# Performance work log

Hardware: AMD Instinct MI355X
Metric: run time of the kernel (lower is better)

Reference implementation:

```python
import jax, jax.numpy as jnp
from jax import lax
import numpy as np

S, B, IN, H, OUT = 101, 16384, 9, 32, 3


def setup_inputs() -> dict:
    key = jax.random.key(0)
    ks = jax.random.split(key, 7)
    s = 1.0 / np.sqrt(H)  # PyTorch LSTM init scale
    return {
        "x": jax.random.normal(ks[0], (S, B, IN), jnp.float32),
        "W_ih": jax.random.uniform(ks[1], (4 * H, IN), jnp.float32, -s, s),
        "W_hh": jax.random.uniform(ks[2], (4 * H, H), jnp.float32, -s, s),
        "b_ih": jax.random.uniform(ks[3], (4 * H,), jnp.float32, -s, s),
        "b_hh": jax.random.uniform(ks[4], (4 * H,), jnp.float32, -s, s),
        "W_lin": jax.random.uniform(ks[5], (OUT, H * S), jnp.float32, -s, s),
        "b_lin": jax.random.uniform(ks[6], (OUT,), jnp.float32, -s, s),
    }


def reference(x, W_ih, W_hh, b_ih, b_hh, W_lin, b_lin):
    seq, batch, _ = x.shape
    hdim = W_hh.shape[1]
    # Precompute input projections for all timesteps: [S, B, 4H]
    x_proj = jnp.einsum('sbi,gi->sbg', x, W_ih) + b_ih + b_hh

    def step(carry, xp_t):
        h, c = carry
        gates = xp_t + h @ W_hh.T  # [B, 4H], PyTorch gate order i,f,g,o
        i, f, g, o = jnp.split(gates, 4, axis=-1)
        c = jax.nn.sigmoid(f) * c + jax.nn.sigmoid(i) * jnp.tanh(g)
        h = jax.nn.sigmoid(o) * jnp.tanh(c)
        return (h, c), h

    h0 = jnp.zeros((batch, hdim), x.dtype)
    (_, _), hs = lax.scan(step, (h0, h0), x_proj)  # hs: [S, B, H]
    # Faithful to the torch code: reshape seq-major output to (-1, H*S)
    flat = hs.reshape(-1, hdim * seq)  # [B, H*S] (seq/batch-interleaved rows)
    return flat @ W_lin.T + b_lin  # [B, OUT]
```

## Files before the change

kernel.cpp:

```cpp
#include <hip/hip_runtime.h>
#include <hip/hip_bf16.h>

#define SEQ   101
#define BATCH 16384
#define INP   9
#define HID   32
#define NOUT  3
#define HSlin 3232
#define SB    (SEQ * BATCH)

typedef __attribute__((ext_vector_type(8))) _Float16 half8;
typedef __attribute__((ext_vector_type(8))) short short8;
typedef __attribute__((ext_vector_type(4))) float f32x4;
typedef __attribute__((ext_vector_type(2))) float f32x2;
typedef __attribute__((ext_vector_type(4))) unsigned u32x4;

#define LOG2E   1.4426950408889634f
#define N2LOG2E (-2.8853900817779268f)

__device__ __forceinline__ unsigned pkh(float a, float b) {
    return __builtin_bit_cast(unsigned, __builtin_amdgcn_cvt_pkrtz(a, b));
}
__device__ __forceinline__ unsigned dpp8u(unsigned v) {
    return (unsigned)__builtin_amdgcn_mov_dpp((int)v, 0x128, 0xF, 0xF, true);
}
__device__ __forceinline__ float dpp8f(float v) {
    return __int_as_float(__builtin_amdgcn_mov_dpp(__float_as_int(v), 0x128, 0xF, 0xF, true));
}

__global__ void prep_kernel(const float* __restrict__ W_ih, const float* __restrict__ W_hh,
                            const float* __restrict__ b_ih, const float* __restrict__ b_hh,
                            unsigned short* __restrict__ whh16, unsigned short* __restrict__ wih16,
                            float* __restrict__ biasc) {
    int tid = threadIdx.x;
    int l   = tid & 63;
    int t   = tid >> 6;
    int row = l & 15;
    int g   = l >> 4;
    int gate = 16 * t + row;
    float sc = ((gate >> 5) == 2) ? (2.f * LOG2E) : LOG2E;
    for (int j = 0; j < 8; ++j) {
        int u = 4 * g + (j & 3) + 16 * (j >> 2);
        _Float16 wh = (_Float16)(W_hh[gate * HID + u] * sc);
        whh16[tid * 8 + j] = __builtin_bit_cast(unsigned short, wh);
        int k = 8 * g + j;
        _Float16 wi = (_Float16)((k < INP) ? (W_ih[gate * INP + k] * sc) : 0.f);
        wih16[tid * 8 + j] = __builtin_bit_cast(unsigned short, wi);
    }
    if (tid < 4 * HID) {
        float bs = ((tid >> 5) == 2) ? (2.f * LOG2E) : LOG2E;
        biasc[tid] = (b_ih[tid] + b_hh[tid]) * bs;
    }
}

template<bool PLANES>
__device__ __forceinline__ void emit_prev(float p0, float p1, float p2,
                                          unsigned psb, float* __restrict__ dataout,
                                          int lane, int cr) {
    p0 += dpp8f(p0);          p1 += dpp8f(p1);          p2 += dpp8f(p2);
    p0 += __shfl_xor(p0, 16); p1 += __shfl_xor(p1, 16); p2 += __shfl_xor(p2, 16);
    p0 += __shfl_xor(p0, 32); p1 += __shfl_xor(p1, 32); p2 += __shfl_xor(p2, 32);
    if (PLANES) {
        if (lane < 8) {
            unsigned blk = psb + (unsigned)lane;
            dataout[0 * SB + blk] = p0;
            dataout[1 * SB + blk] = p1;
            dataout[2 * SB + blk] = p2;
        }
    } else {
        unsigned blk  = psb + (unsigned)cr;
        unsigned r    = blk / 101u;
        unsigned rmin = psb / 101u;
        bool low = (r == rmin);
        float a0 = low ? p0 : 0.f, a1 = low ? p1 : 0.f, a2 = low ? p2 : 0.f;
        float d0 = low ? 0.f : p0, d1 = low ? 0.f : p1, d2 = low ? 0.f : p2;
#pragma unroll
        for (int m = 1; m < 8; m <<= 1) {
            a0 += __shfl_xor(a0, m); a1 += __shfl_xor(a1, m); a2 += __shfl_xor(a2, m);
            d0 += __shfl_xor(d0, m); d1 += __shfl_xor(d1, m); d2 += __shfl_xor(d2, m);
        }
        int anyhi = __any(!low && lane < 8);
        if (lane == 0) {
            atomicAdd(&dataout[rmin * 3 + 0], a0);
            atomicAdd(&dataout[rmin * 3 + 1], a1);
            atomicAdd(&dataout[rmin * 3 + 2], a2);
            if (anyhi) {
                atomicAdd(&dataout[(rmin + 1u) * 3 + 0], d0);
                atomicAdd(&dataout[(rmin + 1u) * 3 + 1], d1);
                atomicAdd(&dataout[(rmin + 1u) * 3 + 2], d2);
            }
        }
    }
}

template<bool PLANES>
__global__ __launch_bounds__(64, 2) void lstm_kernel(
    const float* __restrict__ x,
    const unsigned short* __restrict__ whh_g,
    const unsigned short* __restrict__ wih_g,
    const float* __restrict__ biasc,
    const float* __restrict__ W_lin,
    float* __restrict__ dataout)
{
    const int lane = threadIdx.x;
    const int c    = lane & 15;
    const int cr   = c & 7;
    const bool hi8 = (lane & 8) != 0;
    const int g    = lane >> 4;
    const int b0   = blockIdx.x * 8;
    const int b    = b0 + cr;

    half8 whh[8], xw[8];
    f32x4 biasv[8];
#pragma unroll
    for (int t = 0; t < 8; ++t) {
        whh[t] = __builtin_bit_cast(half8, *reinterpret_cast<const short8*>(whh_g + (t * 64 + lane) * 8));
        xw[t]  = __builtin_bit_cast(half8, *reinterpret_cast<const short8*>(wih_g + (t * 64 + lane) * 8));
        biasv[t] = *reinterpret_cast<const f32x4*>(biasc + 16 * t + 4 * g);
    }

    const bool g0 = (g == 0), g1 = (g == 1);

    f32x2 cs[2] = {{0.f, 0.f}, {0.f, 0.f}};
    f32x2 ho[2] = {{0.f, 0.f}, {0.f, 0.f}};
    u32x4 bhv = {0u, 0u, 0u, 0u};
    float xv[9];
    {
        const float* xp = x + (size_t)b * INP;
#pragma unroll
        for (int i = 0; i < 9; ++i) xv[i] = xp[i];
    }

    float pp0 = 0.f, pp1 = 0.f, pp2 = 0.f;
    unsigned psb = 0;

#pragma unroll 1
    for (int s = 0; s < SEQ; ++s) {
        unsigned blk  = (unsigned)s * BATCH + (unsigned)b;
        unsigned r    = blk / 101u;
        unsigned slot = blk - r * 101u;
        const float* wl = W_lin + slot * HID + 4 * g + (hi8 ? 16 : 0);
        float4 w0 = *(const float4*)(wl);
        float4 w1 = *(const float4*)(wl + HSlin);
        float4 w2 = *(const float4*)(wl + 2 * HSlin);

        short8 xa;
        {
            unsigned x01 = pkh(xv[0], xv[1]), x23 = pkh(xv[2], xv[3]);
            unsigned x45 = pkh(xv[4], xv[5]), x67 = pkh(xv[6], xv[7]);
            unsigned x8z = pkh(xv[8], 0.f);
            u32x4 xt;
            xt[0] = g0 ? x01 : (g1 ? x8z : 0u);
            xt[1] = g0 ? x23 : 0u;
            xt[2] = g0 ? x45 : 0u;
            xt[3] = g0 ? x67 : 0u;
            xa = __builtin_bit_cast(short8, xt);
        }
        half8 bh = __builtin_bit_cast(half8, bhv);

        f32x4 acc[8];
#pragma unroll
        for (int t = 0; t < 8; ++t) {
            acc[t] = __builtin_amdgcn_mfma_f32_16x16x32_f16(xw[t], __builtin_bit_cast(half8, xa), biasv[t], 0, 0, 0);
            acc[t] = __builtin_amdgcn_mfma_f32_16x16x32_f16(whh[t], bh, acc[t], 0, 0, 0);
        }
        if (s > 0) emit_prev<PLANES>(pp0, pp1, pp2, psb, dataout, lane, cr);

        float xn[9];
        if (s < SEQ - 1) {
            const float* xpn = x + ((size_t)(s + 1) * BATCH + b) * INP;
#pragma unroll
            for (int i = 0; i < 9; ++i) xn[i] = xpn[i];
        }

        f32x4 aI = hi8 ? acc[1] : acc[0];
        f32x4 aF = hi8 ? acc[3] : acc[2];
        f32x4 aG = hi8 ? acc[5] : acc[4];
        f32x4 aO = hi8 ? acc[7] : acc[6];
#pragma unroll
        for (int p = 0; p < 2; ++p) {
            f32x2 ef = {__builtin_amdgcn_exp2f(-aF[2*p]), __builtin_amdgcn_exp2f(-aF[2*p+1])};
            f32x2 ei = {__builtin_amdgcn_exp2f(-aI[2*p]), __builtin_amdgcn_exp2f(-aI[2*p+1])};
            f32x2 eg = {__builtin_amdgcn_exp2f(-aG[2*p]), __builtin_amdgcn_exp2f(-aG[2*p+1])};
            f32x2 pf = ef + 1.f;
            f32x2 A  = (ei + 1.f) * (eg + 1.f);
            f32x2 num = cs[p] * A + (1.f - eg) * pf;
            f32x2 den = pf * A;
            f32x2 rd = {__builtin_amdgcn_rcpf(den.x), __builtin_amdgcn_rcpf(den.y)};
            f32x2 cn = num * rd;
            cs[p] = cn;
            f32x2 eo = {__builtin_amdgcn_exp2f(-aO[2*p]), __builtin_amdgcn_exp2f(-aO[2*p+1])};
            f32x2 ec = {__builtin_amdgcn_exp2f(cn.x * N2LOG2E), __builtin_amdgcn_exp2f(cn.y * N2LOG2E)};
            f32x2 dd = (eo + 1.f) * (ec + 1.f);
            f32x2 rh = {__builtin_amdgcn_rcpf(dd.x), __builtin_amdgcn_rcpf(dd.y)};
            ho[p] = (1.f - ec) * rh;
        }
        {
            unsigned oh01 = pkh(ho[0].x, ho[0].y);
            unsigned oh23 = pkh(ho[1].x, ho[1].y);
            unsigned th01 = dpp8u(oh01), th23 = dpp8u(oh23);
            bhv[0] = hi8 ? th01 : oh01;  bhv[1] = hi8 ? th23 : oh23;
            bhv[2] = hi8 ? oh01 : th01;  bhv[3] = hi8 ? oh23 : th23;
        }
        if (s < SEQ - 1) {
#pragma unroll
            for (int i = 0; i < 9; ++i) xv[i] = xn[i];
        }

        pp0 = w0.x * ho[0].x + w0.y * ho[0].y + w0.z * ho[1].x + w0.w * ho[1].y;
        pp1 = w1.x * ho[0].x + w1.y * ho[0].y + w1.z * ho[1].x + w1.w * ho[1].y;
        pp2 = w2.x * ho[0].x + w2.y * ho[0].y + w2.z * ho[1].x + w2.w * ho[1].y;
        psb = (unsigned)s * BATCH + (unsigned)b0;
    }
    emit_prev<PLANES>(pp0, pp1, pp2, psb, dataout, lane, cr);
}

__global__ void finalize_planes(const float* __restrict__ planes, const float* __restrict__ b_lin,
                                float* __restrict__ out) {
    int wid = (blockIdx.x * blockDim.x + threadIdx.x) >> 6;
    int l   = threadIdx.x & 63;
    float v[3];
#pragma unroll
    for (int o = 0; o < 3; ++o) {
        const float* p = planes + (size_t)o * SB + (size_t)wid * 101;
        float t = p[l] + ((l < 37) ? p[l + 64] : 0.f);
#pragma unroll
        for (int m = 1; m < 64; m <<= 1) t += __shfl_xor(t, m);
        v[o] = t;
    }
    if (l == 0) {
        out[wid * 3 + 0] = v[0] + b_lin[0];
        out[wid * 3 + 1] = v[1] + b_lin[1];
        out[wid * 3 + 2] = v[2] + b_lin[2];
    }
}

__global__ void finalize_acc(const float* __restrict__ acc, const float* __restrict__ b_lin,
                             float* __restrict__ out) {
    int i = blockIdx.x * blockDim.x + threadIdx.x;
    if (i < BATCH * NOUT) {
        int r = i / 3;
        int o = i - r * 3;
        out[i] = acc[i] + b_lin[o];
    }
}

extern "C" void kernel_launch(void* const* d_in, const int* in_sizes, int n_in,
                              void* d_out, int out_size, void* d_ws, size_t ws_size,
                              hipStream_t stream) {
    const float* x     = (const float*)d_in[0];
    const float* W_ih  = (const float*)d_in[1];
    const float* W_hh  = (const float*)d_in[2];
    const float* b_ih  = (const float*)d_in[3];
    const float* b_hh  = (const float*)d_in[4];
    const float* W_lin = (const float*)d_in[5];
    const float* b_lin = (const float*)d_in[6];
    float* out = (float*)d_out;

    unsigned short* whh16 = (unsigned short*)d_ws;
    unsigned short* wih16 = whh16 + 4096;
    float* biasc = (float*)(wih16 + 4096);
    float* data  = (float*)((char*)d_ws + 25600);

    size_t need_planes = 25600 + (size_t)3 * SB * sizeof(float);
    bool planes = ws_size >= need_planes;

    hipLaunchKernelGGL(prep_kernel, dim3(1), dim3(512), 0, stream,
                       W_ih, W_hh, b_ih, b_hh, whh16, wih16, biasc);
    if (planes) {
        hipLaunchKernelGGL((lstm_kernel<true>), dim3(BATCH / 8), dim3(64), 0, stream,
                           x, whh16, wih16, biasc, W_lin, data);
        hipLaunchKernelGGL(finalize_planes, dim3(BATCH / 4), dim3(256), 0, stream,
                           data, b_lin, out);
    } else {
        hipMemsetAsync(data, 0, 49160 * sizeof(float), stream);
        hipLaunchKernelGGL((lstm_kernel<false>), dim3(BATCH / 8), dim3(64), 0, stream,
                           x, whh16, wih16, biasc, W_lin, data);
        hipLaunchKernelGGL(finalize_acc, dim3((BATCH * NOUT + 255) / 256), dim3(256), 0, stream,
                           data, b_lin, out);
    }
}
```

Measured before the change: 114.2 us.

## Process 16 batch columns per wave, dropping DPP half-swap of hidden state

Each wave now owns 16 batch elements instead of 8, using the full MFMA N dimension. Each lane computes gate nonlinearities for both hidden halves, so the DPP lane swaps for the h vector and the partial-sum reduction go away. The launch grid halves and launch bounds drop to one wave per SIMD to allow more registers. In exchange, per-lane elementwise work doubles and fewer waves are available to hide the serial recurrence latency.

```diff
diff --git a/kernel.cpp b/kernel.cpp
--- a/kernel.cpp
+++ b/kernel.cpp
@@ -20,12 +20,6 @@
 
 __device__ __forceinline__ unsigned pkh(float a, float b) {
     return __builtin_bit_cast(unsigned, __builtin_amdgcn_cvt_pkrtz(a, b));
-}
-__device__ __forceinline__ unsigned dpp8u(unsigned v) {
-    return (unsigned)__builtin_amdgcn_mov_dpp((int)v, 0x128, 0xF, 0xF, true);
-}
-__device__ __forceinline__ float dpp8f(float v) {
-    return __int_as_float(__builtin_amdgcn_mov_dpp(__float_as_int(v), 0x128, 0xF, 0xF, true));
 }
 
 __global__ void prep_kernel(const float* __restrict__ W_ih, const float* __restrict__ W_hh,
@@ -56,30 +50,29 @@
 template<bool PLANES>
 __device__ __forceinline__ void emit_prev(float p0, float p1, float p2,
                                           unsigned psb, float* __restrict__ dataout,
-                                          int lane, int cr) {
-    p0 += dpp8f(p0);          p1 += dpp8f(p1);          p2 += dpp8f(p2);
+                                          int lane, int c) {
     p0 += __shfl_xor(p0, 16); p1 += __shfl_xor(p1, 16); p2 += __shfl_xor(p2, 16);
     p0 += __shfl_xor(p0, 32); p1 += __shfl_xor(p1, 32); p2 += __shfl_xor(p2, 32);
     if (PLANES) {
-        if (lane < 8) {
+        if (lane < 16) {
             unsigned blk = psb + (unsigned)lane;
             dataout[0 * SB + blk] = p0;
             dataout[1 * SB + blk] = p1;
             dataout[2 * SB + blk] = p2;
         }
     } else {
-        unsigned blk  = psb + (unsigned)cr;
+        unsigned blk  = psb + (unsigned)c;
         unsigned r    = blk / 101u;
         unsigned rmin = psb / 101u;
         bool low = (r == rmin);
         float a0 = low ? p0 : 0.f, a1 = low ? p1 : 0.f, a2 = low ? p2 : 0.f;
         float d0 = low ? 0.f : p0, d1 = low ? 0.f : p1, d2 = low ? 0.f : p2;
 #pragma unroll
-        for (int m = 1; m < 8; m <<= 1) {
+        for (int m = 1; m < 16; m <<= 1) {
             a0 += __shfl_xor(a0, m); a1 += __shfl_xor(a1, m); a2 += __shfl_xor(a2, m);
             d0 += __shfl_xor(d0, m); d1 += __shfl_xor(d1, m); d2 += __shfl_xor(d2, m);
         }
-        int anyhi = __any(!low && lane < 8);
+        int anyhi = __any(!low && lane < 16);
         if (lane == 0) {
             atomicAdd(&dataout[rmin * 3 + 0], a0);
             atomicAdd(&dataout[rmin * 3 + 1], a1);
@@ -94,7 +87,7 @@
 }
 
 template<bool PLANES>
-__global__ __launch_bounds__(64, 2) void lstm_kernel(
+__global__ __launch_bounds__(64, 1) void lstm_kernel(
     const float* __restrict__ x,
     const unsigned short* __restrict__ whh_g,
     const unsigned short* __restrict__ wih_g,
@@ -104,11 +97,9 @@
 {
     const int lane = threadIdx.x;
     const int c    = lane & 15;
-    const int cr   = c & 7;
-    const bool hi8 = (lane & 8) != 0;
     const int g    = lane >> 4;
-    const int b0   = blockIdx.x * 8;
-    const int b    = b0 + cr;
+    const int b0   = blockIdx.x * 16;
+    const int b    = b0 + c;
 
     half8 whh[8], xw[8];
     f32x4 biasv[8];
@@ -121,8 +112,8 @@
 
     const bool g0 = (g == 0), g1 = (g == 1);
 
-    f32x2 cs[2] = {{0.f, 0.f}, {0.f, 0.f}};
-    f32x2 ho[2] = {{0.f, 0.f}, {0.f, 0.f}};
+    f32x2 cs[4] = {{0.f,0.f},{0.f,0.f},{0.f,0.f},{0.f,0.f}};
+    f32x2 hp[4] = {{0.f,0.f},{0.f,0.f},{0.f,0.f},{0.f,0.f}};
     u32x4 bhv = {0u, 0u, 0u, 0u};
     float xv[9];
     {
@@ -139,10 +130,13 @@
         unsigned blk  = (unsigned)s * BATCH + (unsigned)b;
         unsigned r    = blk / 101u;
         unsigned slot = blk - r * 101u;
-        const float* wl = W_lin + slot * HID + 4 * g + (hi8 ? 16 : 0);
-        float4 w0 = *(const float4*)(wl);
-        float4 w1 = *(const float4*)(wl + HSlin);
-        float4 w2 = *(const float4*)(wl + 2 * HSlin);
+        const float* wl = W_lin + slot * HID + 4 * g;
+        float4 w0a = *(const float4*)(wl);
+        float4 w0b = *(const float4*)(wl + 16);
+        float4 w1a = *(const float4*)(wl + HSlin);
+        float4 w1b = *(const float4*)(wl + HSlin + 16);
+        float4 w2a = *(const float4*)(wl + 2 * HSlin);
+        float4 w2b = *(const float4*)(wl + 2 * HSlin + 16);
 
         short8 xa;
         {
@@ -164,7 +158,7 @@
             acc[t] = __builtin_amdgcn_mfma_f32_16x16x32_f16(xw[t], __builtin_bit_cast(half8, xa), biasv[t], 0, 0, 0);
             acc[t] = __builtin_amdgcn_mfma_f32_16x16x32_f16(whh[t], bh, acc[t], 0, 0, 0);
         }
-        if (s > 0) emit_prev<PLANES>(pp0, pp1, pp2, psb, dataout, lane, cr);
+        if (s > 0) emit_prev<PLANES>(pp0, pp1, pp2, psb, dataout, lane, c);
 
         float xn[9];
         if (s < SEQ - 1) {
@@ -173,15 +167,16 @@
             for (int i = 0; i < 9; ++i) xn[i] = xpn[i];
         }
 
-        f32x4 aI = hi8 ? acc[1] : acc[0];
-        f32x4 aF = hi8 ? acc[3] : acc[2];
-        f32x4 aG = hi8 ? acc[5] : acc[4];
-        f32x4 aO = hi8 ? acc[7] : acc[6];
-#pragma unroll
-        for (int p = 0; p < 2; ++p) {
-            f32x2 ef = {__builtin_amdgcn_exp2f(-aF[2*p]), __builtin_amdgcn_exp2f(-aF[2*p+1])};
-            f32x2 ei = {__builtin_amdgcn_exp2f(-aI[2*p]), __builtin_amdgcn_exp2f(-aI[2*p+1])};
-            f32x2 eg = {__builtin_amdgcn_exp2f(-aG[2*p]), __builtin_amdgcn_exp2f(-aG[2*p+1])};
+#pragma unroll
+        for (int p = 0; p < 4; ++p) {
+            const int ht = p >> 1, q0 = 2 * (p & 1);
+            f32x2 aI = {acc[0 + ht][q0], acc[0 + ht][q0 + 1]};
+            f32x2 aF = {acc[2 + ht][q0], acc[2 + ht][q0 + 1]};
+            f32x2 aG = {acc[4 + ht][q0], acc[4 + ht][q0 + 1]};
+            f32x2 aO = {acc[6 + ht][q0], acc[6 + ht][q0 + 1]};
+            f32x2 ef = {__builtin_amdgcn_exp2f(-aF.x), __builtin_amdgcn_exp2f(-aF.y)};
+            f32x2 ei = {__builtin_amdgcn_exp2f(-aI.x), __builtin_amdgcn_exp2f(-aI.y)};
+            f32x2 eg = {__builtin_amdgcn_exp2f(-aG.x), __builtin_amdgcn_exp2f(-aG.y)};
             f32x2 pf = ef + 1.f;
             f32x2 A  = (ei + 1.f) * (eg + 1.f);
             f32x2 num = cs[p] * A + (1.f - eg) * pf;
@@ -189,30 +184,30 @@
             f32x2 rd = {__builtin_amdgcn_rcpf(den.x), __builtin_amdgcn_rcpf(den.y)};
             f32x2 cn = num * rd;
             cs[p] = cn;
-            f32x2 eo = {__builtin_amdgcn_exp2f(-aO[2*p]), __builtin_amdgcn_exp2f(-aO[2*p+1])};
+            f32x2 eo = {__builtin_amdgcn_exp2f(-aO.x), __builtin_amdgcn_exp2f(-aO.y)};
             f32x2 ec = {__builtin_amdgcn_exp2f(cn.x * N2LOG2E), __builtin_amdgcn_exp2f(cn.y * N2LOG2E)};
             f32x2 dd = (eo + 1.f) * (ec + 1.f);
             f32x2 rh = {__builtin_amdgcn_rcpf(dd.x), __builtin_amdgcn_rcpf(dd.y)};
-            ho[p] = (1.f - ec) * rh;
-        }
-        {
-            unsigned oh01 = pkh(ho[0].x, ho[0].y);
-            unsigned oh23 = pkh(ho[1].x, ho[1].y);
-            unsigned th01 = dpp8u(oh01), th23 = dpp8u(oh23);
-            bhv[0] = hi8 ? th01 : oh01;  bhv[1] = hi8 ? th23 : oh23;
-            bhv[2] = hi8 ? oh01 : th01;  bhv[3] = hi8 ? oh23 : th23;
-        }
+            hp[p] = (1.f - ec) * rh;
+        }
+        bhv[0] = pkh(hp[0].x, hp[0].y);
+        bhv[1] = pkh(hp[1].x, hp[1].y);
+        bhv[2] = pkh(hp[2].x, hp[2].y);
+        bhv[3] = pkh(hp[3].x, hp[3].y);
         if (s < SEQ - 1) {
 #pragma unroll
             for (int i = 0; i < 9; ++i) xv[i] = xn[i];
         }
 
-        pp0 = w0.x * ho[0].x + w0.y * ho[0].y + w0.z * ho[1].x + w0.w * ho[1].y;
-        pp1 = w1.x * ho[0].x + w1.y * ho[0].y + w1.z * ho[1].x + w1.w * ho[1].y;
-        pp2 = w2.x * ho[0].x + w2.y * ho[0].y + w2.z * ho[1].x + w2.w * ho[1].y;
+        pp0 = w0a.x*hp[0].x + w0a.y*hp[0].y + w0a.z*hp[1].x + w0a.w*hp[1].y
+            + w0b.x*hp[2].x + w0b.y*hp[2].y + w0b.z*hp[3].x + w0b.w*hp[3].y;
+        pp1 = w1a.x*hp[0].x + w1a.y*hp[0].y + w1a.z*hp[1].x + w1a.w*hp[1].y
+            + w1b.x*hp[2].x + w1b.y*hp[2].y + w1b.z*hp[3].x + w1b.w*hp[3].y;
+        pp2 = w2a.x*hp[0].x + w2a.y*hp[0].y + w2a.z*hp[1].x + w2a.w*hp[1].y
+            + w2b.x*hp[2].x + w2b.y*hp[2].y + w2b.z*hp[3].x + w2b.w*hp[3].y;
         psb = (unsigned)s * BATCH + (unsigned)b0;
     }
-    emit_prev<PLANES>(pp0, pp1, pp2, psb, dataout, lane, cr);
+    emit_prev<PLANES>(pp0, pp1, pp2, psb, dataout, lane, c);
 }
 
 __global__ void finalize_planes(const float* __restrict__ planes, const float* __restrict__ b_lin,
@@ -268,13 +263,13 @@
     hipLaunchKernelGGL(prep_kernel, dim3(1), dim3(512), 0, stream,
                        W_ih, W_hh, b_ih, b_hh, whh16, wih16, biasc);
     if (planes) {
-        hipLaunchKernelGGL((lstm_kernel<true>), dim3(BATCH / 8), dim3(64), 0, stream,
+        hipLaunchKernelGGL((lstm_kernel<true>), dim3(BATCH / 16), dim3(64), 0, stream,
                            x, whh16, wih16, biasc, W_lin, data);
         hipLaunchKernelGGL(finalize_planes, dim3(BATCH / 4), dim3(256), 0, stream,
                            data, b_lin, out);
     } else {
         hipMemsetAsync(data, 0, 49160 * sizeof(float), stream);
-        hipLaunchKernelGGL((lstm_kernel<false>), dim3(BATCH / 8), dim3(64), 0, stream,
+        hipLaunchKernelGGL((lstm_kernel<false>), dim3(BATCH / 16), dim3(64), 0, stream,
                            x, whh16, wih16, biasc, W_lin, data);
         hipLaunchKernelGGL(finalize_acc, dim3((BATCH * NOUT + 255) / 256), dim3(256), 0, stream,
                            data, b_lin, out);
```

New measurement: 150.9 us. +32.1%, slower.

## Software-pipeline the input-projection MFMA one step ahead and strength-reduce slot computation

Applied to the files above, without the earlier changes.

Moves the input-projection MFMA (x·W_ih + bias) out of the recurrent dependency chain by computing it for step s+1 while step s's recurrent MFMA and gate math run, with x loads prefetched two steps ahead. Only the W_hh MFMA now sits on the serial critical path. It also replaces the per-step division by 101 with an incremental modular update (BATCH mod 101 = 22) and uses a shift for s*BATCH. This costs extra registers for the xacc accumulators, which may affect occupancy.

```diff
diff --git a/kernel.cpp b/kernel.cpp
--- a/kernel.cpp
+++ b/kernel.cpp
@@ -124,28 +124,52 @@
     f32x2 cs[2] = {{0.f, 0.f}, {0.f, 0.f}};
     f32x2 ho[2] = {{0.f, 0.f}, {0.f, 0.f}};
     u32x4 bhv = {0u, 0u, 0u, 0u};
+
+    f32x4 xacc[8];
     float xv[9];
     {
         const float* xp = x + (size_t)b * INP;
 #pragma unroll
         for (int i = 0; i < 9; ++i) xv[i] = xp[i];
-    }
+        unsigned x01 = pkh(xv[0], xv[1]), x23 = pkh(xv[2], xv[3]);
+        unsigned x45 = pkh(xv[4], xv[5]), x67 = pkh(xv[6], xv[7]);
+        unsigned x8z = pkh(xv[8], 0.f);
+        u32x4 xt;
+        xt[0] = g0 ? x01 : (g1 ? x8z : 0u);
+        xt[1] = g0 ? x23 : 0u;
+        xt[2] = g0 ? x45 : 0u;
+        xt[3] = g0 ? x67 : 0u;
+        half8 xa = __builtin_bit_cast(half8, xt);
+#pragma unroll
+        for (int t = 0; t < 8; ++t)
+            xacc[t] = __builtin_amdgcn_mfma_f32_16x16x32_f16(xw[t], xa, biasv[t], 0, 0, 0);
+        const float* xp1 = x + ((size_t)BATCH + b) * INP;
+#pragma unroll
+        for (int i = 0; i < 9; ++i) xv[i] = xp1[i];
+    }
+
+    unsigned rr   = (unsigned)b / 101u;
+    unsigned slot = (unsigned)b - rr * 101u;
 
     float pp0 = 0.f, pp1 = 0.f, pp2 = 0.f;
     unsigned psb = 0;
 
 #pragma unroll 1
     for (int s = 0; s < SEQ; ++s) {
-        unsigned blk  = (unsigned)s * BATCH + (unsigned)b;
-        unsigned r    = blk / 101u;
-        unsigned slot = blk - r * 101u;
         const float* wl = W_lin + slot * HID + 4 * g + (hi8 ? 16 : 0);
         float4 w0 = *(const float4*)(wl);
         float4 w1 = *(const float4*)(wl + HSlin);
         float4 w2 = *(const float4*)(wl + 2 * HSlin);
 
-        short8 xa;
-        {
+        half8 bh = __builtin_bit_cast(half8, bhv);
+        f32x4 acc[8];
+#pragma unroll
+        for (int t = 0; t < 8; ++t)
+            acc[t] = __builtin_amdgcn_mfma_f32_16x16x32_f16(whh[t], bh, xacc[t], 0, 0, 0);
+
+        if (s > 0) emit_prev<PLANES>(pp0, pp1, pp2, psb, dataout, lane, cr);
+
+        if (s + 1 < SEQ) {
             unsigned x01 = pkh(xv[0], xv[1]), x23 = pkh(xv[2], xv[3]);
             unsigned x45 = pkh(xv[4], xv[5]), x67 = pkh(xv[6], xv[7]);
             unsigned x8z = pkh(xv[8], 0.f);
@@ -154,21 +178,14 @@
             xt[1] = g0 ? x23 : 0u;
             xt[2] = g0 ? x45 : 0u;
             xt[3] = g0 ? x67 : 0u;
-            xa = __builtin_bit_cast(short8, xt);
-        }
-        half8 bh = __builtin_bit_cast(half8, bhv);
-
-        f32x4 acc[8];
-#pragma unroll
-        for (int t = 0; t < 8; ++t) {
-            acc[t] = __builtin_amdgcn_mfma_f32_16x16x32_f16(xw[t], __builtin_bit_cast(half8, xa), biasv[t], 0, 0, 0);
-            acc[t] = __builtin_amdgcn_mfma_f32_16x16x32_f16(whh[t], bh, acc[t], 0, 0, 0);
-        }
-        if (s > 0) emit_prev<PLANES>(pp0, pp1, pp2, psb, dataout, lane, cr);
-
+            half8 xa = __builtin_bit_cast(half8, xt);
+#pragma unroll
+            for (int t = 0; t < 8; ++t)
+                xacc[t] = __builtin_amdgcn_mfma_f32_16x16x32_f16(xw[t], xa, biasv[t], 0, 0, 0);
+        }
         float xn[9];
-        if (s < SEQ - 1) {
-            const float* xpn = x + ((size_t)(s + 1) * BATCH + b) * INP;
+        if (s + 2 < SEQ) {
+            const float* xpn = x + ((size_t)(s + 2) * BATCH + b) * INP;
 #pragma unroll
             for (int i = 0; i < 9; ++i) xn[i] = xpn[i];
         }
@@ -202,7 +219,7 @@
             bhv[0] = hi8 ? th01 : oh01;  bhv[1] = hi8 ? th23 : oh23;
             bhv[2] = hi8 ? oh01 : th01;  bhv[3] = hi8 ? oh23 : th23;
         }
-        if (s < SEQ - 1) {
+        if (s + 2 < SEQ) {
 #pragma unroll
             for (int i = 0; i < 9; ++i) xv[i] = xn[i];
         }
@@ -210,7 +227,10 @@
         pp0 = w0.x * ho[0].x + w0.y * ho[0].y + w0.z * ho[1].x + w0.w * ho[1].y;
         pp1 = w1.x * ho[0].x + w1.y * ho[0].y + w1.z * ho[1].x + w1.w * ho[1].y;
         pp2 = w2.x * ho[0].x + w2.y * ho[0].y + w2.z * ho[1].x + w2.w * ho[1].y;
-        psb = (unsigned)s * BATCH + (unsigned)b0;
+        psb = ((unsigned)s << 14) + (unsigned)b0;
+
+        slot += 22u;
+        slot = (slot >= 101u) ? (slot - 101u) : slot;
     }
     emit_prev<PLANES>(pp0, pp1, pp2, psb, dataout, lane, cr);
 }
```

Result: slower. 117.1 us (+2.5%).
